# Performance work log

Measured on AMD Instinct MI355X. Metric: run time of the kernel, lower is better.

Reference implementation:

```python
import jax, jax.numpy as jnp
import numpy as np

MEAN = 0.0
STD = 0.04
STEP = 2

def setup_inputs() -> dict:
    key = jax.random.key(0)
    k1, k2 = jax.random.split(key)
    B, L = 512, 100000
    x = jax.random.normal(k1, (B, L), dtype=jnp.float32)
    noise = jax.random.normal(k2, (L,), dtype=jnp.float32)
    move = 100  # deterministic stand-in for RandomLoopMove's random shift
    return {"x": x, "noise": noise, "move": move}

def reference(x, noise, move):
    B, L = x.shape
    # LoopMove: circular shift along the trace axis
    x = jnp.roll(x, move, axis=1)
    # AddGaussianNoise: single noise vector (randn*std + mean) added to every row
    x = x + (noise * STD + MEAN)
    # Integrate(step=2, mode='mean'): segment-mean over non-overlapping windows,
    # each pooled value written to positions 2j and 2j+1 (exactly fills the trace)
    pooled = jnp.mean(x.reshape(B, L // STEP, STEP), axis=2)  # [B, L/2]
    x = jnp.repeat(pooled, STEP, axis=1)                      # [B, L]
    # Normalize: per-row standardization (np.std uses ddof=0)
    mu = jnp.mean(x, axis=1, keepdims=True)
    sd = jnp.std(x, axis=1, keepdims=True)
    return (x - mu) / sd
```

## Files before the change

kernel.cpp:

```cpp
#include <hip/hip_runtime.h>


#define THREADS 1024
#define NWAVES (THREADS / 64)
#define KMAX 25

typedef float f32x4 __attribute__((ext_vector_type(4)));

__device__ __forceinline__ void row_stats(
    float sum, float sq, int tid, int J,
    float* s_sum, float* s_sq, float* s_mu, float* s_isd,
    float& mu, float& isd)
{
    #pragma unroll
    for (int off = 32; off > 0; off >>= 1) {
        sum += __shfl_down(sum, off, 64);
        sq  += __shfl_down(sq,  off, 64);
    }
    const int wave = tid >> 6;
    if ((tid & 63) == 0) { s_sum[wave] = sum; s_sq[wave] = sq; }
    __syncthreads();
    if (tid == 0) {
        float ts = 0.f, tq = 0.f;
        #pragma unroll
        for (int w = 0; w < NWAVES; ++w) { ts += s_sum[w]; tq += s_sq[w]; }
        float invJ = 1.0f / (float)J;
        float m   = ts * invJ;
        float var = tq * invJ - m * m;
        *s_mu  = m;
        *s_isd = rsqrtf(fmaxf(var, 1e-30f));
    }
    __syncthreads();
    mu  = *s_mu;
    isd = *s_isd;
}

__device__ __forceinline__ void generic_row(
    const float* __restrict__ xrow, const float* __restrict__ noise,
    float* __restrict__ orow, int L, int mv, int tid,
    float* s_sum, float* s_sq, float* s_mu, float* s_isd)
{
    const int J = L >> 1;
    const bool fast2 = ((mv & 1) == 0) && ((L & 1) == 0);
    float sum = 0.f, sq = 0.f;
    for (int j = tid; j < J; j += THREADS) {
        int s = 2 * j - mv; if (s < 0) s += L;
        float a, c;
        if (fast2) { float2 v = *(const float2*)(xrow + s); a = v.x; c = v.y; }
        else { int s1 = s + 1; if (s1 >= L) s1 -= L; a = xrow[s]; c = xrow[s1]; }
        float2 nv = *(const float2*)(noise + 2 * j);
        float p = 0.5f * (a + c + 0.04f * (nv.x + nv.y));
        sum += p; sq += p * p;
    }
    float mu, isd;
    row_stats(sum, sq, tid, J, s_sum, s_sq, s_mu, s_isd, mu, isd);
    for (int j = tid; j < J; j += THREADS) {
        int s = 2 * j - mv; if (s < 0) s += L;
        float a, c;
        if (fast2) { float2 v = *(const float2*)(xrow + s); a = v.x; c = v.y; }
        else { int s1 = s + 1; if (s1 >= L) s1 -= L; a = xrow[s]; c = xrow[s1]; }
        float2 nv = *(const float2*)(noise + 2 * j);
        float p = 0.5f * (a + c + 0.04f * (nv.x + nv.y));
        float r = (p - mu) * isd;
        *(float2*)(orow + 2 * j) = make_float2(r, r);
    }
}

__global__ __launch_bounds__(THREADS) void tbt_pipe(
    const float* __restrict__ x,
    const float* __restrict__ noise,
    const int* __restrict__ movep,
    float* __restrict__ out,
    int L)
{
    const int tid = threadIdx.x;
    const int J = L >> 1;
    const int U = J >> 1;

    int mv = movep[0];
    mv %= L; if (mv < 0) mv += L;

    const size_t roff = (size_t)(2 * blockIdx.x) * (size_t)L;
    const float* __restrict__ xr0 = x + roff;
    const float* __restrict__ xr1 = xr0 + L;
    float* __restrict__ or0 = out + roff;
    float* __restrict__ or1 = or0 + L;

    __shared__ float s_sum[NWAVES], s_sq[NWAVES];
    __shared__ float s_stat[4];

    const bool fast4 = ((mv & 3) == 0) && ((L & 3) == 0);
    if (!fast4) {
        generic_row(xr0, noise, or0, L, mv, tid, s_sum, s_sq, &s_stat[0], &s_stat[1]);
        __syncthreads();
        generic_row(xr1, noise, or1, L, mv, tid, s_sum, s_sq, &s_stat[2], &s_stat[3]);
        return;
    }

    float p0[2 * KMAX], p1[2 * KMAX];
    float sum = 0.f, sq = 0.f;

    #pragma unroll
    for (int k = 0; k < KMAX; ++k) {
        const int u = tid + k * THREADS;
        if (u < U) {
            int s = 4 * u - mv; if (s < 0) s += L;
            f32x4 v = __builtin_nontemporal_load((const f32x4*)(xr0 + s));
            float4 n = *(const float4*)(noise + 4 * u);
            float a = 0.5f * (v.x + v.y) + 0.02f * (n.x + n.y);
            float c = 0.5f * (v.z + v.w) + 0.02f * (n.z + n.w);
            p0[2 * k]     = a;
            p0[2 * k + 1] = c;
            sum += a + c;
            sq  += a * a + c * c;
        }
    }
    float mu0, isd0;
    row_stats(sum, sq, tid, J, s_sum, s_sq, &s_stat[0], &s_stat[1], mu0, isd0);

    sum = 0.f; sq = 0.f;
    #pragma unroll
    for (int k = 0; k < KMAX; ++k) {
        const int u = tid + k * THREADS;
        if (u < U) {
            int s = 4 * u - mv; if (s < 0) s += L;
            f32x4 v = __builtin_nontemporal_load((const f32x4*)(xr1 + s));
            float4 n = *(const float4*)(noise + 4 * u);
            float ra = (p0[2 * k]     - mu0) * isd0;
            float rc = (p0[2 * k + 1] - mu0) * isd0;
            f32x4 o = {ra, ra, rc, rc};
            __builtin_nontemporal_store(o, (f32x4*)(or0 + 4 * u));
            float a = 0.5f * (v.x + v.y) + 0.02f * (n.x + n.y);
            float c = 0.5f * (v.z + v.w) + 0.02f * (n.z + n.w);
            p1[2 * k]     = a;
            p1[2 * k + 1] = c;
            sum += a + c;
            sq  += a * a + c * c;
        }
    }
    float mu1, isd1;
    row_stats(sum, sq, tid, J, s_sum, s_sq, &s_stat[2], &s_stat[3], mu1, isd1);

    #pragma unroll
    for (int k = 0; k < KMAX; ++k) {
        const int u = tid + k * THREADS;
        if (u < U) {
            float ra = (p1[2 * k]     - mu1) * isd1;
            float rc = (p1[2 * k + 1] - mu1) * isd1;
            f32x4 o = {ra, ra, rc, rc};
            __builtin_nontemporal_store(o, (f32x4*)(or1 + 4 * u));
        }
    }
}


__global__ __launch_bounds__(THREADS) void tbt_kernel(
    const float* __restrict__ x,
    const float* __restrict__ noise,
    const int* __restrict__ movep,
    float* __restrict__ out,
    int L)
{
    const int b   = blockIdx.x;
    const int tid = threadIdx.x;
    const int J   = L >> 1;

    int mv = movep[0];
    mv %= L; if (mv < 0) mv += L;

    const float* __restrict__ xrow = x + (size_t)b * (size_t)L;
    float* __restrict__ orow       = out + (size_t)b * (size_t)L;

    const bool fast4 = ((mv & 3) == 0) && ((L & 3) == 0);

    const int U  = J >> 1;
    const int nk = (U + THREADS - 1) / THREADS;

    __shared__ float s_sum[NWAVES], s_sq[NWAVES];
    __shared__ float s_stat[2];

    if (fast4 && nk <= KMAX) {
        float p[2 * KMAX];
        float sum = 0.f, sq = 0.f;

        #pragma unroll
        for (int k = 0; k < KMAX; ++k) {
            const int u = tid + k * THREADS;
            if (u < U) {
                int s = 4 * u - mv; if (s < 0) s += L;
                f32x4 v = __builtin_nontemporal_load((const f32x4*)(xrow + s));
                float4 n = *(const float4*)(noise + 4 * u);
                float a = 0.5f * (v.x + v.y) + 0.02f * (n.x + n.y);
                float c = 0.5f * (v.z + v.w) + 0.02f * (n.z + n.w);
                p[2 * k]     = a;
                p[2 * k + 1] = c;
                sum += a + c;
                sq  += a * a + c * c;
            }
        }

        float mu, isd;
        row_stats(sum, sq, tid, J, s_sum, s_sq, &s_stat[0], &s_stat[1], mu, isd);

        #pragma unroll
        for (int k = 0; k < KMAX; ++k) {
            const int u = tid + k * THREADS;
            if (u < U) {
                float ra = (p[2 * k]     - mu) * isd;
                float rc = (p[2 * k + 1] - mu) * isd;
                f32x4 o = {ra, ra, rc, rc};
                __builtin_nontemporal_store(o, (f32x4*)(orow + 4 * u));
            }
        }
        return;
    }

    generic_row(xrow, noise, orow, L, mv, tid, s_sum, s_sq, &s_stat[0], &s_stat[1]);
}

extern "C" void kernel_launch(void* const* d_in, const int* in_sizes, int n_in,
                              void* d_out, int out_size, void* d_ws, size_t ws_size,
                              hipStream_t stream) {
    const float* x     = (const float*)d_in[0];
    const float* noise = (const float*)d_in[1];
    const int*   move  = (const int*)d_in[2];
    float*       out   = (float*)d_out;

    const int L = in_sizes[1];
    const int B = in_sizes[0] / L;

    const int J  = L >> 1;
    const int U  = J >> 1;
    const int nk = (U + THREADS - 1) / THREADS;

    if (((L & 3) == 0) && ((B & 1) == 0) && nk <= KMAX && B >= 2) {
        tbt_pipe<<<B / 2, THREADS, 0, stream>>>(x, noise, move, out, L);
    } else {
        tbt_kernel<<<B, THREADS, 0, stream>>>(x, noise, move, out, L);
    }
}
```

Measured before the change: 336.5 us.

## Replace two-row pipelined block with one-row-per-block templated kernel

```diff
diff --git a/kernel.cpp b/kernel.cpp
--- a/kernel.cpp
+++ b/kernel.cpp
@@ -66,7 +66,8 @@
     }
 }
 
-__global__ __launch_bounds__(THREADS) void tbt_pipe(
+template<int KFULL>
+__global__ __launch_bounds__(THREADS, 4) void tbt_row(
     const float* __restrict__ x,
     const float* __restrict__ noise,
     const int* __restrict__ movep,
@@ -80,75 +81,68 @@
     int mv = movep[0];
     mv %= L; if (mv < 0) mv += L;
 
-    const size_t roff = (size_t)(2 * blockIdx.x) * (size_t)L;
-    const float* __restrict__ xr0 = x + roff;
-    const float* __restrict__ xr1 = xr0 + L;
-    float* __restrict__ or0 = out + roff;
-    float* __restrict__ or1 = or0 + L;
+    const size_t roff = (size_t)blockIdx.x * (size_t)L;
+    const float* __restrict__ xrow = x + roff;
+    float* __restrict__ orow       = out + roff;
 
     __shared__ float s_sum[NWAVES], s_sq[NWAVES];
-    __shared__ float s_stat[4];
+    __shared__ float s_stat[2];
 
     const bool fast4 = ((mv & 3) == 0) && ((L & 3) == 0);
     if (!fast4) {
-        generic_row(xr0, noise, or0, L, mv, tid, s_sum, s_sq, &s_stat[0], &s_stat[1]);
-        __syncthreads();
-        generic_row(xr1, noise, or1, L, mv, tid, s_sum, s_sq, &s_stat[2], &s_stat[3]);
+        generic_row(xrow, noise, orow, L, mv, tid, s_sum, s_sq, &s_stat[0], &s_stat[1]);
         return;
     }
 
-    float p0[2 * KMAX], p1[2 * KMAX];
+    float p[2 * (KFULL + 1)];
     float sum = 0.f, sq = 0.f;
 
     #pragma unroll
-    for (int k = 0; k < KMAX; ++k) {
+    for (int k = 0; k < KFULL; ++k) {
         const int u = tid + k * THREADS;
+        int s = 4 * u - mv; if (s < 0) s += L;
+        f32x4 v = __builtin_nontemporal_load((const f32x4*)(xrow + s));
+        float4 n = *(const float4*)(noise + 4 * u);
+        float a = 0.5f * (v.x + v.y) + 0.02f * (n.x + n.y);
+        float c = 0.5f * (v.z + v.w) + 0.02f * (n.z + n.w);
+        p[2 * k]     = a;
+        p[2 * k + 1] = c;
+        sum += a + c;
+        sq  += a * a + c * c;
+    }
+    {
+        const int u = tid + KFULL * THREADS;
         if (u < U) {
             int s = 4 * u - mv; if (s < 0) s += L;
-            f32x4 v = __builtin_nontemporal_load((const f32x4*)(xr0 + s));
+            f32x4 v = __builtin_nontemporal_load((const f32x4*)(xrow + s));
             float4 n = *(const float4*)(noise + 4 * u);
             float a = 0.5f * (v.x + v.y) + 0.02f * (n.x + n.y);
             float c = 0.5f * (v.z + v.w) + 0.02f * (n.z + n.w);
-            p0[2 * k]     = a;
-            p0[2 * k + 1] = c;
+            p[2 * KFULL]     = a;
+            p[2 * KFULL + 1] = c;
             sum += a + c;
             sq  += a * a + c * c;
         }
     }
-    float mu0, isd0;
-    row_stats(sum, sq, tid, J, s_sum, s_sq, &s_stat[0], &s_stat[1], mu0, isd0);
-
-    sum = 0.f; sq = 0.f;
+
+    float mu, isd;
+    row_stats(sum, sq, tid, J, s_sum, s_sq, &s_stat[0], &s_stat[1], mu, isd);
+
     #pragma unroll
-    for (int k = 0; k < KMAX; ++k) {
+    for (int k = 0; k < KFULL; ++k) {
         const int u = tid + k * THREADS;
+        float ra = (p[2 * k]     - mu) * isd;
+        float rc = (p[2 * k + 1] - mu) * isd;
+        f32x4 o = {ra, ra, rc, rc};
+        __builtin_nontemporal_store(o, (f32x4*)(orow + 4 * u));
+    }
+    {
+        const int u = tid + KFULL * THREADS;
         if (u < U) {
-            int s = 4 * u - mv; if (s < 0) s += L;
-            f32x4 v = __builtin_nontemporal_load((const f32x4*)(xr1 + s));
-            float4 n = *(const float4*)(noise + 4 * u);
-            float ra = (p0[2 * k]     - mu0) * isd0;
-            float rc = (p0[2 * k + 1] - mu0) * isd0;
+            float ra = (p[2 * KFULL]     - mu) * isd;
+            float rc = (p[2 * KFULL + 1] - mu) * isd;
             f32x4 o = {ra, ra, rc, rc};
-            __builtin_nontemporal_store(o, (f32x4*)(or0 + 4 * u));
-            float a = 0.5f * (v.x + v.y) + 0.02f * (n.x + n.y);
-            float c = 0.5f * (v.z + v.w) + 0.02f * (n.z + n.w);
-            p1[2 * k]     = a;
-            p1[2 * k + 1] = c;
-            sum += a + c;
-            sq  += a * a + c * c;
-        }
-    }
-    float mu1, isd1;
-    row_stats(sum, sq, tid, J, s_sum, s_sq, &s_stat[2], &s_stat[3], mu1, isd1);
-
-    #pragma unroll
-    for (int k = 0; k < KMAX; ++k) {
-        const int u = tid + k * THREADS;
-        if (u < U) {
-            float ra = (p1[2 * k]     - mu1) * isd1;
-            float rc = (p1[2 * k + 1] - mu1) * isd1;
-            f32x4 o = {ra, ra, rc, rc};
-            __builtin_nontemporal_store(o, (f32x4*)(or1 + 4 * u));
+            __builtin_nontemporal_store(o, (f32x4*)(orow + 4 * u));
         }
     }
 }
@@ -231,10 +225,10 @@
 
     const int J  = L >> 1;
     const int U  = J >> 1;
-    const int nk = (U + THREADS - 1) / THREADS;
-
-    if (((L & 3) == 0) && ((B & 1) == 0) && nk <= KMAX && B >= 2) {
-        tbt_pipe<<<B / 2, THREADS, 0, stream>>>(x, noise, move, out, L);
+    const int KF = U / THREADS;
+
+    if (((L & 3) == 0) && KF == 24 && U <= 25 * THREADS) {
+        tbt_row<24><<<B, THREADS, 0, stream>>>(x, noise, move, out, L);
     } else {
         tbt_kernel<<<B, THREADS, 0, stream>>>(x, noise, move, out, L);
     }
```

New measurement: 348.6 us. +3.6%, slower.
